# Kernel optimization log

Hardware: AMD Instinct MI355X
Metric: run time of the kernel (lower is better)

Reference implementation:

```python
import jax, jax.numpy as jnp
import numpy as np

N, D_IN, D_HID, D_OUT, E = 8192, 1024, 4096, 1024, 8
N_ACTIVE = max(1, int(E * 0.625))  # 5
TEMP = float(np.e)               # temperature = np.e in source


def setup_inputs() -> dict:
    key = jax.random.key(0)
    ks = jax.random.split(key, 4)
    return {
        "x": jax.random.normal(ks[0], (N, D_IN), jnp.float32),
        "gate_w": jax.random.normal(ks[1], (D_IN, E), jnp.float32) * 0.02,
        "gate_b": jnp.zeros((E,), jnp.float32),
        "w1": jax.random.normal(ks[2], (E, D_IN, D_HID), jnp.float32) * 0.02,
        "b1": jnp.zeros((E, D_HID), jnp.float32),
        "w2": jax.random.normal(ks[3], (E, D_HID, D_OUT), jnp.float32) * 0.02,
        "b2": jnp.zeros((E, D_OUT), jnp.float32),
    }


def reference(x, gate_w, gate_b, w1, b1, w2, b2):
    # Gate: softmax over experts at temperature e, then top-k mask + renormalize
    scores = (x @ gate_w + gate_b) / TEMP                 # [N, E]
    probs = jax.nn.softmax(scores, axis=-1)               # [N, E]
    _, topk_idx = jax.lax.top_k(probs, N_ACTIVE)          # [N, k]
    mask = jax.nn.one_hot(topk_idx, E, dtype=probs.dtype).sum(axis=-2)  # [N, E]
    weights = probs * mask
    weights = weights / (weights.sum(axis=-1, keepdims=True) + 1e-8)
    # Dense all-experts FFN (dropout is eval-mode identity)
    h = jax.nn.relu(jnp.einsum('nd,edh->neh', x, w1) + b1)   # [N, E, d_hid]
    e_out = jnp.einsum('neh,eho->neo', h, w2) + b2           # [N, E, d_out]
    # Camp A (first E/2 experts) added, camp G subtracted: out = out_a - out_g
    sign = jnp.where(jnp.arange(E) < E // 2, 1.0, -1.0)      # [E]
    return jnp.einsum('ne,neo->no', weights * sign, e_out)   # [N, d_out]
```

## Files before the change

### kernel.cpp

```cpp
#include <hip/hip_runtime.h>
#include <hip/hip_bf16.h>
#include <cmath>


typedef _Float16 f16;
typedef _Float16 f16x8 __attribute__((ext_vector_type(8)));
typedef _Float16 f16x4 __attribute__((ext_vector_type(4)));
typedef float f32x4 __attribute__((ext_vector_type(4)));

#define NROWS 8192
#define DIN   1024
#define DHID  4096
#define DOUT  1024
#define NEXP  8

#define OFF_SGATE 0u
#define OFF_XH    262144u
#define OFF_W1T   17039360u
#define OFF_W2T   84148224u
#define OFF_P1    151257088u
#define OFF_HH    184811520u
#define NEED_NE2  319029248ull

__device__ __forceinline__ void gload_lds16(const void* gsrc, void* ldsdst) {
  __builtin_amdgcn_global_load_lds(
      (const __attribute__((address_space(1))) unsigned int*)gsrc,
      (__attribute__((address_space(3))) unsigned int*)ldsdst, 16, 0, 0);
}

__global__ void gate_kernel(const float* __restrict__ x,
                            const float* __restrict__ gw,
                            const float* __restrict__ gb,
                            float* __restrict__ sgate) {
  const int row = blockIdx.x * 4 + (threadIdx.x >> 6);
  const int l = threadIdx.x & 63;
  const float* xr = x + (size_t)row * DIN;
  float acc[8] = {0.f,0.f,0.f,0.f,0.f,0.f,0.f,0.f};
#pragma unroll
  for (int j = 0; j < 16; ++j) {
    const int k = l + 64 * j;
    const float xv = xr[k];
    const float4 g0 = *(const float4*)(gw + (size_t)k * 8);
    const float4 g1 = *(const float4*)(gw + (size_t)k * 8 + 4);
    acc[0] += xv * g0.x; acc[1] += xv * g0.y; acc[2] += xv * g0.z; acc[3] += xv * g0.w;
    acc[4] += xv * g1.x; acc[5] += xv * g1.y; acc[6] += xv * g1.z; acc[7] += xv * g1.w;
  }
#pragma unroll
  for (int off = 32; off > 0; off >>= 1) {
#pragma unroll
    for (int e = 0; e < 8; ++e) acc[e] += __shfl_xor(acc[e], off, 64);
  }
  if (l == 0) {
    const float invT = 0.36787944117144233f;
    float p[8]; float mx = -1e30f;
#pragma unroll
    for (int e = 0; e < 8; ++e) { p[e] = (acc[e] + gb[e]) * invT; mx = fmaxf(mx, p[e]); }
    float S = 0.f;
#pragma unroll
    for (int e = 0; e < 8; ++e) { p[e] = expf(p[e] - mx); S += p[e]; }
    const float inv = 1.0f / S;
#pragma unroll
    for (int e = 0; e < 8; ++e) p[e] *= inv;
    bool keep[8] = {true,true,true,true,true,true,true,true};
    for (int t = 0; t < 3; ++t) {
      float pmin = 1e30f; int mi = -1;
      for (int e = 0; e < 8; ++e)
        if (keep[e] && (p[e] < pmin || (p[e] == pmin && e > mi))) { pmin = p[e]; mi = e; }
      keep[mi] = false;
    }
    float wsum = 0.f;
#pragma unroll
    for (int e = 0; e < 8; ++e) if (keep[e]) wsum += p[e];
    const float rinv = 1.0f / (wsum + 1e-8f);
#pragma unroll
    for (int e = 0; e < 8; ++e) {
      const float wv = keep[e] ? p[e] * rinv : 0.0f;
      sgate[(size_t)row * 8 + e] = (e < 4) ? wv : -wv;
    }
  }
}

__global__ void cvt_x_kernel(const float* __restrict__ x, f16* __restrict__ xh) {
  const size_t i = ((size_t)blockIdx.x * blockDim.x + threadIdx.x) * 4;
  const float4 v = *(const float4*)(x + i);
  f16x4 o = { (f16)v.x, (f16)v.y, (f16)v.z, (f16)v.w };
  *(f16x4*)(xh + i) = o;
}

__global__ void transpose_cvt(const float* __restrict__ in, f16* __restrict__ out,
                              int R, int C) {
  __shared__ float tile[32][33];
  const int e = blockIdx.z;
  const float* ine = in + (size_t)e * R * C;
  f16* oute = out + (size_t)e * R * C;
  const int c0 = blockIdx.x * 32, r0 = blockIdx.y * 32;
  const int tx = threadIdx.x, ty = threadIdx.y;
#pragma unroll
  for (int i = 0; i < 4; ++i)
    tile[ty + i * 8][tx] = ine[(size_t)(r0 + ty + i * 8) * C + c0 + tx];
  __syncthreads();
#pragma unroll
  for (int i = 0; i < 4; ++i)
    oute[(size_t)(c0 + ty + i * 8) * R + r0 + tx] = (f16)tile[tx][ty + i * 8];
}

#define MFMAOP(a_, b_, c_) __builtin_amdgcn_mfma_f32_16x16x32_f16(a_, b_, c_, 0, 0, 0)

template <int EPI>
__global__ __launch_bounds__(512, 2) void gemm8p(
    const f16* __restrict__ A, int lda,
    const f16* __restrict__ B, int ldb, int nt,
    long long khA, long long khB,
    const float* __restrict__ bias,
    f16* __restrict__ outH, int ldc,
    float* outP0, float* outP1, int p1w,
    const float* __restrict__ sgate, int expert, int gx) {
  __shared__ alignas(16) f16 lA[4 * 8192];
  __shared__ alignas(16) f16 lB[4 * 8192];
  const int tid = threadIdx.x;
  const int l = tid & 63, w = tid >> 6;
  const int wr = w >> 2, wc = w & 3;

  const int nwg = gridDim.x, cpx = nwg >> 3;
  const int lg = ((int)blockIdx.x & 7) * cpx + ((int)blockIdx.x >> 3);

  int m0, n0;
  const f16* Aeff = A;
  const f16* Beff = B;
  float* P = nullptr;
  bool pw = false;
  if constexpr (EPI == 1) {
    const int xcd = lg / cpx;
    const int cc = lg - xcd * cpx;
    const int nper = gx >> 3;
    m0 = (cc / nper) * 256;
    n0 = (xcd * nper + (cc % nper)) * 256;
  } else {
    const int xx = lg >> 5, cc = lg & 31;
    const int kh = xx >> 2;
    n0 = (xx & 3) * 256;
    m0 = cc * 256;
    Aeff = A + (size_t)kh * (size_t)khA;
    Beff = B + (size_t)kh * (size_t)khB;
    P = kh ? outP1 : outP0;
    pw = (p1w != 0);
  }

  const int srow = tid >> 3;
  const int sxc = (tid & 7) ^ (srow & 7);
  const f16* pA = Aeff + (size_t)(m0 + srow) * lda + sxc * 8;
  const f16* pB = Beff + (size_t)(n0 + srow) * ldb + sxc * 8;
  f16* const dA = lA + w * 512;
  f16* const dB = lB + w * 512;

#define STG_A(slot, h, tk) do { \
    const f16* s_ = pA + (size_t)(h) * 128 * lda + (size_t)(tk) * 64; \
    gload_lds16(s_,            dA + (slot) * 8192); \
    gload_lds16(s_ + 64 * lda, dA + (slot) * 8192 + 4096); \
  } while (0)
#define STG_B(slot, h, tk) do { \
    const f16* s_ = pB + (size_t)(h) * 128 * ldb + (size_t)(tk) * 64; \
    gload_lds16(s_,            dB + (slot) * 8192); \
    gload_lds16(s_ + 64 * ldb, dB + (slot) * 8192 + 4096); \
  } while (0)

  const int cg = l >> 4, xr = l & 7;
  const int ok0 = ((cg ^ xr) << 4);
  const int ok1 = (((4 + cg) ^ xr) << 4);
  const char* const baA = (const char*)lA + (l & 15) * 128;
  const char* const baB = (const char*)lB + (wc & 1) * 8192 + (l & 15) * 128;

#define RDA(CA, f, o) (*(const f16x8*)(baA + ((CA) + wr) * 16384 + (f) * 2048 + (o)))
#define RDB(CB, g, o) (*(const f16x8*)(baB + ((CB) + (wc >> 1)) * 16384 + (g) * 2048 + (o)))

#define SYNC() do { __builtin_amdgcn_sched_barrier(0); \
    __builtin_amdgcn_s_barrier(); \
    __builtin_amdgcn_sched_barrier(0); } while (0)
#define ENDPH() do { __builtin_amdgcn_s_setprio(0); \
    __builtin_amdgcn_sched_barrier(0); \
    __builtin_amdgcn_s_barrier(); \
    __builtin_amdgcn_sched_barrier(0); } while (0)
#define VM6() do { __builtin_amdgcn_sched_barrier(0); \
    asm volatile("s_waitcnt vmcnt(6)"); \
    __builtin_amdgcn_sched_barrier(0); } while (0)
#define VM0() do { __builtin_amdgcn_sched_barrier(0); \
    asm volatile("s_waitcnt vmcnt(0)"); \
    __builtin_amdgcn_sched_barrier(0); } while (0)
#define MM(f, g, ar, br) acc[f][g] = MFMAOP(ar, br, acc[f][g])

  f32x4 acc[8][4] = {};
  f16x8 fa0, fa1, fa2, fa3;
  f16x8 ga0, ga1, ga2, ga3;
  f16x8 b00, b10, b20, b30;
  f16x8 b01, b11, b21, b31;

#define TILEBODY(T, CA, CB, SB1, SB0n, SA0n, SA1n) do { \
     \
    fa0 = RDA(CA, 0, ok0); fa1 = RDA(CA, 1, ok0); \
    fa2 = RDA(CA, 2, ok0); fa3 = RDA(CA, 3, ok0); \
    b00 = RDB(CB, 0, ok0); b10 = RDB(CB, 1, ok0); \
    b20 = RDB(CB, 2, ok0); b30 = RDB(CB, 3, ok0); \
    if ((T) + 1 < nt) STG_B(SB1, 1, (T) + 1); \
    SYNC(); \
    __builtin_amdgcn_s_setprio(1); \
    MM(0,0,fa0,b00); MM(0,1,fa0,b10); MM(0,2,fa0,b20); MM(0,3,fa0,b30); \
    MM(1,0,fa1,b00); MM(1,1,fa1,b10); MM(1,2,fa1,b20); MM(1,3,fa1,b30); \
    MM(2,0,fa2,b00); MM(2,1,fa2,b10); MM(2,2,fa2,b20); MM(2,3,fa2,b30); \
    MM(3,0,fa3,b00); MM(3,1,fa3,b10); MM(3,2,fa3,b20); MM(3,3,fa3,b30); \
    ENDPH(); \
     \
    ga0 = RDA(CA, 0, ok1); ga1 = RDA(CA, 1, ok1); \
    ga2 = RDA(CA, 2, ok1); ga3 = RDA(CA, 3, ok1); \
    b01 = RDB(CB, 0, ok1); b11 = RDB(CB, 1, ok1); \
    b21 = RDB(CB, 2, ok1); b31 = RDB(CB, 3, ok1); \
    SYNC(); \
    __builtin_amdgcn_s_setprio(1); \
    MM(0,0,ga0,b01); MM(0,1,ga0,b11); MM(0,2,ga0,b21); MM(0,3,ga0,b31); \
    MM(1,0,ga1,b01); MM(1,1,ga1,b11); MM(1,2,ga1,b21); MM(1,3,ga1,b31); \
    MM(2,0,ga2,b01); MM(2,1,ga2,b11); MM(2,2,ga2,b21); MM(2,3,ga2,b31); \
    MM(3,0,ga3,b01); MM(3,1,ga3,b11); MM(3,2,ga3,b21); MM(3,3,ga3,b31); \
    ENDPH(); \
     \
    fa0 = RDA(CA, 4, ok0); fa1 = RDA(CA, 5, ok0); \
    fa2 = RDA(CA, 6, ok0); fa3 = RDA(CA, 7, ok0); \
    ga0 = RDA(CA, 4, ok1); ga1 = RDA(CA, 5, ok1); \
    ga2 = RDA(CA, 6, ok1); ga3 = RDA(CA, 7, ok1); \
    if ((T) + 2 < nt) STG_B(SB0n, 0, (T) + 2); \
    SYNC(); \
    __builtin_amdgcn_s_setprio(1); \
    MM(4,0,fa0,b00); MM(4,1,fa0,b10); MM(4,2,fa0,b20); MM(4,3,fa0,b30); \
    MM(5,0,fa1,b00); MM(5,1,fa1,b10); MM(5,2,fa1,b20); MM(5,3,fa1,b30); \
    MM(6,0,fa2,b00); MM(6,1,fa2,b10); MM(6,2,fa2,b20); MM(6,3,fa2,b30); \
    MM(7,0,fa3,b00); MM(7,1,fa3,b10); MM(7,2,fa3,b20); MM(7,3,fa3,b30); \
    ENDPH(); \
     \
    if ((T) + 2 < nt) { STG_A(SA0n, 0, (T) + 2); STG_A(SA1n, 1, (T) + 2); \
                        VM6(); } \
    else { VM0(); } \
    SYNC(); \
    __builtin_amdgcn_s_setprio(1); \
    MM(4,0,ga0,b01); MM(4,1,ga0,b11); MM(4,2,ga0,b21); MM(4,3,ga0,b31); \
    MM(5,0,ga1,b01); MM(5,1,ga1,b11); MM(5,2,ga1,b21); MM(5,3,ga1,b31); \
    MM(6,0,ga2,b01); MM(6,1,ga2,b11); MM(6,2,ga2,b21); MM(6,3,ga2,b31); \
    MM(7,0,ga3,b01); MM(7,1,ga3,b11); MM(7,2,ga3,b21); MM(7,3,ga3,b31); \
    ENDPH(); \
  } while (0)

  STG_A(0, 0, 0); STG_B(0, 0, 0); STG_A(1, 1, 0); STG_B(1, 1, 0);
  STG_A(2, 0, 1); STG_B(2, 0, 1); STG_A(3, 1, 1);
  __builtin_amdgcn_sched_barrier(0);
  asm volatile("s_waitcnt vmcnt(6)");
  __builtin_amdgcn_sched_barrier(0);
  __builtin_amdgcn_s_barrier();
  __builtin_amdgcn_sched_barrier(0);

  for (int t = 0; t < nt; t += 2) {
    TILEBODY(t,     0, 0, 3, 0, 0, 1);
    TILEBODY(t + 1, 2, 2, 1, 2, 2, 3);
  }
  __builtin_amdgcn_sched_barrier(0);
  asm volatile("s_waitcnt vmcnt(0)");
  __builtin_amdgcn_sched_barrier(0);

  if constexpr (EPI == 1) {
#pragma unroll
    for (int mi = 0; mi < 8; ++mi)
#pragma unroll
      for (int r = 0; r < 4; ++r) {
        const int row = m0 + wr * 128 + mi * 16 + (l >> 4) * 4 + r;
        const float sg = sgate[(size_t)row * 8 + expert];
#pragma unroll
        for (int ni = 0; ni < 4; ++ni) {
          const int col = n0 + wc * 64 + ni * 16 + (l & 15);
          const float v = acc[mi][ni][r] + bias[col];
          outH[(size_t)row * ldc + col] = (f16)(fmaxf(v, 0.0f) * sg);
        }
      }
  } else {
    float* const scr = (w < 4) ? (float*)lA + w * 4096
                               : (float*)lB + (w - 4) * 4096;
    const int hl = l >> 4, ll = l & 15;
#pragma unroll
    for (int p = 0; p < 2; ++p) {
#pragma unroll
      for (int mi4 = 0; mi4 < 4; ++mi4)
#pragma unroll
        for (int r = 0; r < 4; ++r) {
          const int rowl = mi4 * 16 + hl * 4 + r;
#pragma unroll
          for (int ni = 0; ni < 4; ++ni)
            scr[rowl * 64 + ni * 16 + ll] = acc[p * 4 + mi4][ni][r];
        }
#pragma unroll
      for (int i = 0; i < 16; ++i) {
        const int rowl = hl + i * 4;
        f32x4 v = *(const f32x4*)(scr + rowl * 64 + ll * 4);
        const int row = m0 + wr * 128 + p * 64 + rowl;
        const int col = n0 + wc * 64 + ll * 4;
        f32x4* gp = (f32x4*)(P + (size_t)row * 1024 + col);
        if (!pw) {
          const f32x4 g = *gp;
          v[0] += g[0]; v[1] += g[1]; v[2] += g[2]; v[3] += g[3];
        }
        *gp = v;
      }
    }
  }
#undef STG_A
#undef STG_B
#undef RDA
#undef RDB
#undef SYNC
#undef ENDPH
#undef VM6
#undef VM0
#undef MM
#undef TILEBODY
}

template <bool WITHP>
__global__ void finalize_out(const float* p0,
                             const float* __restrict__ p1,
                             const float* __restrict__ sgate,
                             const float* __restrict__ b2,
                             float* out) {
  const int i = blockIdx.x * 256 + threadIdx.x;
  const int n = i >> 8, c4 = i & 255;
  float4 a = make_float4(0.f, 0.f, 0.f, 0.f);
  if constexpr (WITHP) {
    const float4 u = ((const float4*)p0)[i];
    const float4 v = ((const float4*)p1)[i];
    a.x = u.x + v.x; a.y = u.y + v.y; a.z = u.z + v.z; a.w = u.w + v.w;
  }
  const float* sg = sgate + (size_t)n * 8;
#pragma unroll
  for (int e = 0; e < 8; ++e) {
    const float s = sg[e];
    const float4 bv = ((const float4*)(b2 + (size_t)e * 1024))[c4];
    a.x += s * bv.x; a.y += s * bv.y; a.z += s * bv.z; a.w += s * bv.w;
  }
  ((float4*)out)[i] = a;
}

extern "C" void kernel_launch(void* const* d_in, const int* in_sizes, int n_in,
                              void* d_out, int out_size, void* d_ws, size_t ws_size,
                              hipStream_t stream) {
  const float* x  = (const float*)d_in[0];
  const float* gw = (const float*)d_in[1];
  const float* gb = (const float*)d_in[2];
  const float* w1 = (const float*)d_in[3];
  const float* b1 = (const float*)d_in[4];
  const float* w2 = (const float*)d_in[5];
  const float* b2 = (const float*)d_in[6];
  float* out = (float*)d_out;

  char* ws = (char*)d_ws;
  float* sgate = (float*)(ws + OFF_SGATE);
  f16* xh  = (f16*)(ws + OFF_XH);
  f16* w1t = (f16*)(ws + OFF_W1T);
  f16* w2t = (f16*)(ws + OFF_W2T);
  float* p1 = (float*)(ws + OFF_P1);
  f16* hh  = (f16*)(ws + OFF_HH);

  const int NE = (ws_size >= NEED_NE2) ? 2 : 1;
  const int ngrp = NEXP / NE;

  gate_kernel<<<NROWS / 4, 256, 0, stream>>>(x, gw, gb, sgate);
  cvt_x_kernel<<<(NROWS * DIN) / (256 * 4), 256, 0, stream>>>(x, xh);
  transpose_cvt<<<dim3(DHID / 32, DIN / 32, NEXP), dim3(32, 8), 0, stream>>>(w1, w1t, DIN, DHID);
  transpose_cvt<<<dim3(DOUT / 32, DHID / 32, NEXP), dim3(32, 8), 0, stream>>>(w2, w2t, DHID, DOUT);

  const long long khA = (long long)NE * 2048;
  const long long khB = (NE == 2) ? (long long)DOUT * DHID
                                  : 2048LL;
  const int nt2 = NE * 32;
  for (int g = 0; g < ngrp; ++g) {
    for (int ei = 0; ei < NE; ++ei) {
      const int e = g * NE + ei;
      gemm8p<1><<<512, 512, 0, stream>>>(
          xh, DIN, w1t + (size_t)e * DHID * DIN, DIN, DIN / 64,
          0, 0,
          b1 + (size_t)e * DHID, hh + (size_t)ei * DHID, NE * DHID,
          nullptr, nullptr, 0, sgate, e, DHID / 256);
    }
    gemm8p<2><<<256, 512, 0, stream>>>(
        hh, NE * DHID, w2t + (size_t)g * NE * DOUT * DHID, DHID, nt2,
        khA, khB,
        nullptr, nullptr, 0, out, p1, (g == 0) ? 1 : 0, nullptr, 0, 0);
  }
  finalize_out<true><<<(NROWS * DOUT) / (256 * 4), 256, 0, stream>>>(
      out, p1, sgate, b2, out);
}
```

Baseline: 1.442 ms.

## Software-pipeline LDS fragment reads one phase ahead of MFMA in GEMM mainloop

Restructures the GEMM inner loop so the LDS reads for the next phase are issued before the current phase's MFMAs. This adds more fragment registers (16 A-fragment registers instead of 8), and the first fragments of the next tile are prefetched after the end-of-tile barrier. Several of the block barriers before compute phases are removed or replaced with lgkmcnt waits. The goal is to hide LDS read latency behind matrix-core work and cut barrier stalls. The cost is higher VGPR pressure, which may lower occupancy, and a subtler synchronisation scheme that has to stay race-free.

```diff
diff --git a/kernel.cpp b/kernel.cpp
--- a/kernel.cpp
+++ b/kernel.cpp
@@ -173,94 +173,98 @@
 #define RDA(CA, f, o) (*(const f16x8*)(baA + ((CA) + wr) * 16384 + (f) * 2048 + (o)))
 #define RDB(CB, g, o) (*(const f16x8*)(baB + ((CB) + (wc >> 1)) * 16384 + (g) * 2048 + (o)))
 
-#define SYNC() do { __builtin_amdgcn_sched_barrier(0); \
-    __builtin_amdgcn_s_barrier(); \
-    __builtin_amdgcn_sched_barrier(0); } while (0)
-#define ENDPH() do { __builtin_amdgcn_s_setprio(0); \
-    __builtin_amdgcn_sched_barrier(0); \
-    __builtin_amdgcn_s_barrier(); \
-    __builtin_amdgcn_sched_barrier(0); } while (0)
-#define VM6() do { __builtin_amdgcn_sched_barrier(0); \
-    asm volatile("s_waitcnt vmcnt(6)"); \
-    __builtin_amdgcn_sched_barrier(0); } while (0)
-#define VM0() do { __builtin_amdgcn_sched_barrier(0); \
-    asm volatile("s_waitcnt vmcnt(0)"); \
-    __builtin_amdgcn_sched_barrier(0); } while (0)
+#define SB0() __builtin_amdgcn_sched_barrier(0)
+#define ENDPH() do { __builtin_amdgcn_s_setprio(0); SB0(); \
+    __builtin_amdgcn_s_barrier(); SB0(); } while (0)
+#define LGKM0() do { SB0(); asm volatile("s_waitcnt lgkmcnt(0)"); SB0(); } while (0)
+#define VM6() do { SB0(); asm volatile("s_waitcnt vmcnt(6)"); SB0(); } while (0)
+#define VM0() do { SB0(); asm volatile("s_waitcnt vmcnt(0)"); SB0(); } while (0)
 #define MM(f, g, ar, br) acc[f][g] = MFMAOP(ar, br, acc[f][g])
 
   f32x4 acc[8][4] = {};
-  f16x8 fa0, fa1, fa2, fa3;
-  f16x8 ga0, ga1, ga2, ga3;
+  f16x8 a00, a01, a02, a03;
+  f16x8 a10, a11, a12, a13;
+  f16x8 a20, a21, a22, a23;
+  f16x8 a30, a31, a32, a33;
   f16x8 b00, b10, b20, b30;
   f16x8 b01, b11, b21, b31;
 
-#define TILEBODY(T, CA, CB, SB1, SB0n, SA0n, SA1n) do { \
+#define TILEBODY(T, CA, CB, SB1, SB0n, SA0n, SA1n, CAn, CBn) do { \
      \
-    fa0 = RDA(CA, 0, ok0); fa1 = RDA(CA, 1, ok0); \
-    fa2 = RDA(CA, 2, ok0); fa3 = RDA(CA, 3, ok0); \
-    b00 = RDB(CB, 0, ok0); b10 = RDB(CB, 1, ok0); \
-    b20 = RDB(CB, 2, ok0); b30 = RDB(CB, 3, ok0); \
     if ((T) + 1 < nt) STG_B(SB1, 1, (T) + 1); \
-    SYNC(); \
+    a10 = RDA(CA, 0, ok1); a11 = RDA(CA, 1, ok1); \
+    a12 = RDA(CA, 2, ok1); a13 = RDA(CA, 3, ok1); \
+    b01 = RDB(CB, 0, ok1); b11 = RDB(CB, 1, ok1); \
+    b21 = RDB(CB, 2, ok1); b31 = RDB(CB, 3, ok1); \
+    SB0(); \
     __builtin_amdgcn_s_setprio(1); \
-    MM(0,0,fa0,b00); MM(0,1,fa0,b10); MM(0,2,fa0,b20); MM(0,3,fa0,b30); \
-    MM(1,0,fa1,b00); MM(1,1,fa1,b10); MM(1,2,fa1,b20); MM(1,3,fa1,b30); \
-    MM(2,0,fa2,b00); MM(2,1,fa2,b10); MM(2,2,fa2,b20); MM(2,3,fa2,b30); \
-    MM(3,0,fa3,b00); MM(3,1,fa3,b10); MM(3,2,fa3,b20); MM(3,3,fa3,b30); \
+    MM(0,0,a00,b00); MM(0,1,a00,b10); MM(0,2,a00,b20); MM(0,3,a00,b30); \
+    MM(1,0,a01,b00); MM(1,1,a01,b10); MM(1,2,a01,b20); MM(1,3,a01,b30); \
+    MM(2,0,a02,b00); MM(2,1,a02,b10); MM(2,2,a02,b20); MM(2,3,a02,b30); \
+    MM(3,0,a03,b00); MM(3,1,a03,b10); MM(3,2,a03,b20); MM(3,3,a03,b30); \
     ENDPH(); \
      \
-    ga0 = RDA(CA, 0, ok1); ga1 = RDA(CA, 1, ok1); \
-    ga2 = RDA(CA, 2, ok1); ga3 = RDA(CA, 3, ok1); \
-    b01 = RDB(CB, 0, ok1); b11 = RDB(CB, 1, ok1); \
-    b21 = RDB(CB, 2, ok1); b31 = RDB(CB, 3, ok1); \
-    SYNC(); \
+    a20 = RDA(CA, 4, ok0); a21 = RDA(CA, 5, ok0); \
+    a22 = RDA(CA, 6, ok0); a23 = RDA(CA, 7, ok0); \
+    a30 = RDA(CA, 4, ok1); a31 = RDA(CA, 5, ok1); \
+    a32 = RDA(CA, 6, ok1); a33 = RDA(CA, 7, ok1); \
+    SB0(); \
     __builtin_amdgcn_s_setprio(1); \
-    MM(0,0,ga0,b01); MM(0,1,ga0,b11); MM(0,2,ga0,b21); MM(0,3,ga0,b31); \
-    MM(1,0,ga1,b01); MM(1,1,ga1,b11); MM(1,2,ga1,b21); MM(1,3,ga1,b31); \
-    MM(2,0,ga2,b01); MM(2,1,ga2,b11); MM(2,2,ga2,b21); MM(2,3,ga2,b31); \
-    MM(3,0,ga3,b01); MM(3,1,ga3,b11); MM(3,2,ga3,b21); MM(3,3,ga3,b31); \
+    MM(0,0,a10,b01); MM(0,1,a10,b11); MM(0,2,a10,b21); MM(0,3,a10,b31); \
+    MM(1,0,a11,b01); MM(1,1,a11,b11); MM(1,2,a11,b21); MM(1,3,a11,b31); \
+    MM(2,0,a12,b01); MM(2,1,a12,b11); MM(2,2,a12,b21); MM(2,3,a12,b31); \
+    MM(3,0,a13,b01); MM(3,1,a13,b11); MM(3,2,a13,b21); MM(3,3,a13,b31); \
     ENDPH(); \
      \
-    fa0 = RDA(CA, 4, ok0); fa1 = RDA(CA, 5, ok0); \
-    fa2 = RDA(CA, 6, ok0); fa3 = RDA(CA, 7, ok0); \
-    ga0 = RDA(CA, 4, ok1); ga1 = RDA(CA, 5, ok1); \
-    ga2 = RDA(CA, 6, ok1); ga3 = RDA(CA, 7, ok1); \
     if ((T) + 2 < nt) STG_B(SB0n, 0, (T) + 2); \
-    SYNC(); \
+    LGKM0(); \
     __builtin_amdgcn_s_setprio(1); \
-    MM(4,0,fa0,b00); MM(4,1,fa0,b10); MM(4,2,fa0,b20); MM(4,3,fa0,b30); \
-    MM(5,0,fa1,b00); MM(5,1,fa1,b10); MM(5,2,fa1,b20); MM(5,3,fa1,b30); \
-    MM(6,0,fa2,b00); MM(6,1,fa2,b10); MM(6,2,fa2,b20); MM(6,3,fa2,b30); \
-    MM(7,0,fa3,b00); MM(7,1,fa3,b10); MM(7,2,fa3,b20); MM(7,3,fa3,b30); \
+    MM(4,0,a20,b00); MM(4,1,a20,b10); MM(4,2,a20,b20); MM(4,3,a20,b30); \
+    MM(5,0,a21,b00); MM(5,1,a21,b10); MM(5,2,a21,b20); MM(5,3,a21,b30); \
+    MM(6,0,a22,b00); MM(6,1,a22,b10); MM(6,2,a22,b20); MM(6,3,a22,b30); \
+    MM(7,0,a23,b00); MM(7,1,a23,b10); MM(7,2,a23,b20); MM(7,3,a23,b30); \
     ENDPH(); \
      \
     if ((T) + 2 < nt) { STG_A(SA0n, 0, (T) + 2); STG_A(SA1n, 1, (T) + 2); \
                         VM6(); } \
     else { VM0(); } \
-    SYNC(); \
+    __builtin_amdgcn_s_barrier(); \
+    SB0(); \
+    if ((T) + 1 < nt) { \
+      a00 = RDA(CAn, 0, ok0); a01 = RDA(CAn, 1, ok0); \
+      a02 = RDA(CAn, 2, ok0); a03 = RDA(CAn, 3, ok0); \
+      b00 = RDB(CBn, 0, ok0); b10 = RDB(CBn, 1, ok0); \
+      b20 = RDB(CBn, 2, ok0); b30 = RDB(CBn, 3, ok0); \
+    } \
+    SB0(); \
     __builtin_amdgcn_s_setprio(1); \
-    MM(4,0,ga0,b01); MM(4,1,ga0,b11); MM(4,2,ga0,b21); MM(4,3,ga0,b31); \
-    MM(5,0,ga1,b01); MM(5,1,ga1,b11); MM(5,2,ga1,b21); MM(5,3,ga1,b31); \
-    MM(6,0,ga2,b01); MM(6,1,ga2,b11); MM(6,2,ga2,b21); MM(6,3,ga2,b31); \
-    MM(7,0,ga3,b01); MM(7,1,ga3,b11); MM(7,2,ga3,b21); MM(7,3,ga3,b31); \
+    MM(4,0,a30,b01); MM(4,1,a30,b11); MM(4,2,a30,b21); MM(4,3,a30,b31); \
+    MM(5,0,a31,b01); MM(5,1,a31,b11); MM(5,2,a31,b21); MM(5,3,a31,b31); \
+    MM(6,0,a32,b01); MM(6,1,a32,b11); MM(6,2,a32,b21); MM(6,3,a32,b31); \
+    MM(7,0,a33,b01); MM(7,1,a33,b11); MM(7,2,a33,b21); MM(7,3,a33,b31); \
     ENDPH(); \
   } while (0)
 
   STG_A(0, 0, 0); STG_B(0, 0, 0); STG_A(1, 1, 0); STG_B(1, 1, 0);
   STG_A(2, 0, 1); STG_B(2, 0, 1); STG_A(3, 1, 1);
-  __builtin_amdgcn_sched_barrier(0);
+  SB0();
   asm volatile("s_waitcnt vmcnt(6)");
-  __builtin_amdgcn_sched_barrier(0);
+  SB0();
   __builtin_amdgcn_s_barrier();
-  __builtin_amdgcn_sched_barrier(0);
+  SB0();
+  a00 = RDA(0, 0, ok0); a01 = RDA(0, 1, ok0);
+  a02 = RDA(0, 2, ok0); a03 = RDA(0, 3, ok0);
+  b00 = RDB(0, 0, ok0); b10 = RDB(0, 1, ok0);
+  b20 = RDB(0, 2, ok0); b30 = RDB(0, 3, ok0);
+  SB0();
 
   for (int t = 0; t < nt; t += 2) {
-    TILEBODY(t,     0, 0, 3, 0, 0, 1);
-    TILEBODY(t + 1, 2, 2, 1, 2, 2, 3);
-  }
-  __builtin_amdgcn_sched_barrier(0);
+    TILEBODY(t,     0, 0, 3, 0, 0, 1, 2, 2);
+    TILEBODY(t + 1, 2, 2, 1, 2, 2, 3, 0, 0);
+  }
+  SB0();
   asm volatile("s_waitcnt vmcnt(0)");
-  __builtin_amdgcn_sched_barrier(0);
+  SB0();
 
   if constexpr (EPI == 1) {
 #pragma unroll
@@ -310,8 +314,9 @@
 #undef STG_B
 #undef RDA
 #undef RDB
-#undef SYNC
+#undef SB0
 #undef ENDPH
+#undef LGKM0
 #undef VM6
 #undef VM0
 #undef MM
```

After: 1.976 ms. +37.0%, slower.

## Route only top-k selected tokens through each expert via gathered indices

Applied to the files above, without the earlier changes.

The gate kernel now builds per-expert token index lists with atomic counters. Each expert's first GEMM gathers only its selected rows and skips tiles beyond the padded count, and the second GEMM scatter-adds into output rows. Since each token keeps 5 of 8 experts, this cuts matmul work relative to dense all-expert compute. It adds a zero-init pass, atomics, non-contiguous row gathers and read-modify-write scatter accumulation, and it drops the two-expert batching path.

```diff
diff --git a/kernel.cpp b/kernel.cpp
--- a/kernel.cpp
+++ b/kernel.cpp
@@ -15,12 +15,13 @@
 #define NEXP  8
 
 #define OFF_SGATE 0u
-#define OFF_XH    262144u
-#define OFF_W1T   17039360u
-#define OFF_W2T   84148224u
-#define OFF_P1    151257088u
-#define OFF_HH    184811520u
-#define NEED_NE2  319029248ull
+#define OFF_CNT   262144u
+#define OFF_IDX   266240u
+#define OFF_XH    528384u
+#define OFF_W1T   17305600u
+#define OFF_W2T   84414464u
+#define OFF_P1    151523328u
+#define OFF_HH    185077760u
 
 __device__ __forceinline__ void gload_lds16(const void* gsrc, void* ldsdst) {
   __builtin_amdgcn_global_load_lds(
@@ -28,10 +29,21 @@
       (__attribute__((address_space(3))) unsigned int*)ldsdst, 16, 0, 0);
 }
 
+__global__ void zero_init(float* __restrict__ out, float* __restrict__ p1,
+                          int* __restrict__ cnt) {
+  const size_t i = (size_t)blockIdx.x * 256 + threadIdx.x;
+  const float4 z = make_float4(0.f, 0.f, 0.f, 0.f);
+  ((float4*)out)[i] = z;
+  ((float4*)p1)[i] = z;
+  if (blockIdx.x == 0 && threadIdx.x < 8) cnt[threadIdx.x] = 0;
+}
+
 __global__ void gate_kernel(const float* __restrict__ x,
                             const float* __restrict__ gw,
                             const float* __restrict__ gb,
-                            float* __restrict__ sgate) {
+                            float* __restrict__ sgate,
+                            int* __restrict__ cnt,
+                            int* __restrict__ idx) {
   const int row = blockIdx.x * 4 + (threadIdx.x >> 6);
   const int l = threadIdx.x & 63;
   const float* xr = x + (size_t)row * DIN;
@@ -77,6 +89,11 @@
       const float wv = keep[e] ? p[e] * rinv : 0.0f;
       sgate[(size_t)row * 8 + e] = (e < 4) ? wv : -wv;
     }
+    for (int e = 0; e < 8; ++e)
+      if (keep[e]) {
+        const int pos = atomicAdd(&cnt[e], 1);
+        idx[e * NROWS + pos] = row;
+      }
   }
 }
 
@@ -110,10 +127,10 @@
 __global__ __launch_bounds__(512, 2) void gemm8p(
     const f16* __restrict__ A, int lda,
     const f16* __restrict__ B, int ldb, int nt,
-    long long khA, long long khB,
+    const int* __restrict__ idx_e, const int* __restrict__ cntp,
     const float* __restrict__ bias,
     f16* __restrict__ outH, int ldc,
-    float* outP0, float* outP1, int p1w,
+    float* outP0, float* outP1,
     const float* __restrict__ sgate, int expert, int gx) {
   __shared__ alignas(16) f16 lA[4 * 8192];
   __shared__ alignas(16) f16 lB[4 * 8192];
@@ -124,11 +141,13 @@
   const int nwg = gridDim.x, cpx = nwg >> 3;
   const int lg = ((int)blockIdx.x & 7) * cpx + ((int)blockIdx.x >> 3);
 
+  const int Me = cntp[expert];
+  const int Mpad = (Me + 255) & ~255;
+
   int m0, n0;
   const f16* Aeff = A;
   const f16* Beff = B;
   float* P = nullptr;
-  bool pw = false;
   if constexpr (EPI == 1) {
     const int xcd = lg / cpx;
     const int cc = lg - xcd * cpx;
@@ -140,23 +159,36 @@
     const int kh = xx >> 2;
     n0 = (xx & 3) * 256;
     m0 = cc * 256;
-    Aeff = A + (size_t)kh * (size_t)khA;
-    Beff = B + (size_t)kh * (size_t)khB;
+    Aeff = A + kh * 2048;
+    Beff = B + kh * 2048;
     P = kh ? outP1 : outP0;
-    pw = (p1w != 0);
-  }
+  }
+  if (m0 >= Mpad) return;
 
   const int srow = tid >> 3;
   const int sxc = (tid & 7) ^ (srow & 7);
-  const f16* pA = Aeff + (size_t)(m0 + srow) * lda + sxc * 8;
+  const f16 *pA00, *pA01, *pA10, *pA11;
+  if constexpr (EPI == 1) {
+    const int r00 = m0 + srow,       r01 = m0 + 64 + srow;
+    const int r10 = m0 + 128 + srow, r11 = m0 + 192 + srow;
+    pA00 = A + (size_t)((r00 < Me) ? idx_e[r00] : 0) * lda + sxc * 8;
+    pA01 = A + (size_t)((r01 < Me) ? idx_e[r01] : 0) * lda + sxc * 8;
+    pA10 = A + (size_t)((r10 < Me) ? idx_e[r10] : 0) * lda + sxc * 8;
+    pA11 = A + (size_t)((r11 < Me) ? idx_e[r11] : 0) * lda + sxc * 8;
+  } else {
+    pA00 = Aeff + (size_t)(m0 + srow) * lda + sxc * 8;
+    pA01 = pA00 + (size_t)64 * lda;
+    pA10 = pA00 + (size_t)128 * lda;
+    pA11 = pA00 + (size_t)192 * lda;
+  }
   const f16* pB = Beff + (size_t)(n0 + srow) * ldb + sxc * 8;
   f16* const dA = lA + w * 512;
   f16* const dB = lB + w * 512;
 
 #define STG_A(slot, h, tk) do { \
-    const f16* s_ = pA + (size_t)(h) * 128 * lda + (size_t)(tk) * 64; \
-    gload_lds16(s_,            dA + (slot) * 8192); \
-    gload_lds16(s_ + 64 * lda, dA + (slot) * 8192 + 4096); \
+    const size_t kb = (size_t)(tk) * 64; \
+    gload_lds16(((h) ? pA10 : pA00) + kb, dA + (slot) * 8192); \
+    gload_lds16(((h) ? pA11 : pA01) + kb, dA + (slot) * 8192 + 4096); \
   } while (0)
 #define STG_B(slot, h, tk) do { \
     const f16* s_ = pB + (size_t)(h) * 128 * ldb + (size_t)(tk) * 64; \
@@ -173,19 +205,12 @@
 #define RDA(CA, f, o) (*(const f16x8*)(baA + ((CA) + wr) * 16384 + (f) * 2048 + (o)))
 #define RDB(CB, g, o) (*(const f16x8*)(baB + ((CB) + (wc >> 1)) * 16384 + (g) * 2048 + (o)))
 
-#define SYNC() do { __builtin_amdgcn_sched_barrier(0); \
-    __builtin_amdgcn_s_barrier(); \
-    __builtin_amdgcn_sched_barrier(0); } while (0)
-#define ENDPH() do { __builtin_amdgcn_s_setprio(0); \
-    __builtin_amdgcn_sched_barrier(0); \
-    __builtin_amdgcn_s_barrier(); \
-    __builtin_amdgcn_sched_barrier(0); } while (0)
-#define VM6() do { __builtin_amdgcn_sched_barrier(0); \
-    asm volatile("s_waitcnt vmcnt(6)"); \
-    __builtin_amdgcn_sched_barrier(0); } while (0)
-#define VM0() do { __builtin_amdgcn_sched_barrier(0); \
-    asm volatile("s_waitcnt vmcnt(0)"); \
-    __builtin_amdgcn_sched_barrier(0); } while (0)
+#define SB0() __builtin_amdgcn_sched_barrier(0)
+#define SYNC() do { SB0(); __builtin_amdgcn_s_barrier(); SB0(); } while (0)
+#define ENDPH() do { __builtin_amdgcn_s_setprio(0); SB0(); \
+    __builtin_amdgcn_s_barrier(); SB0(); } while (0)
+#define VM6() do { SB0(); asm volatile("s_waitcnt vmcnt(6)"); SB0(); } while (0)
+#define VM0() do { SB0(); asm volatile("s_waitcnt vmcnt(0)"); SB0(); } while (0)
 #define MM(f, g, ar, br) acc[f][g] = MFMAOP(ar, br, acc[f][g])
 
   f32x4 acc[8][4] = {};
@@ -248,32 +273,33 @@
 
   STG_A(0, 0, 0); STG_B(0, 0, 0); STG_A(1, 1, 0); STG_B(1, 1, 0);
   STG_A(2, 0, 1); STG_B(2, 0, 1); STG_A(3, 1, 1);
-  __builtin_amdgcn_sched_barrier(0);
+  SB0();
   asm volatile("s_waitcnt vmcnt(6)");
-  __builtin_amdgcn_sched_barrier(0);
+  SB0();
   __builtin_amdgcn_s_barrier();
-  __builtin_amdgcn_sched_barrier(0);
+  SB0();
 
   for (int t = 0; t < nt; t += 2) {
     TILEBODY(t,     0, 0, 3, 0, 0, 1);
     TILEBODY(t + 1, 2, 2, 1, 2, 2, 3);
   }
-  __builtin_amdgcn_sched_barrier(0);
+  SB0();
   asm volatile("s_waitcnt vmcnt(0)");
-  __builtin_amdgcn_sched_barrier(0);
+  SB0();
 
   if constexpr (EPI == 1) {
 #pragma unroll
     for (int mi = 0; mi < 8; ++mi)
 #pragma unroll
       for (int r = 0; r < 4; ++r) {
-        const int row = m0 + wr * 128 + mi * 16 + (l >> 4) * 4 + r;
-        const float sg = sgate[(size_t)row * 8 + expert];
+        const int slot = m0 + wr * 128 + mi * 16 + (l >> 4) * 4 + r;
+        const int grow = (slot < Me) ? idx_e[slot] : 0;
+        const float sg = sgate[(size_t)grow * 8 + expert];
 #pragma unroll
         for (int ni = 0; ni < 4; ++ni) {
           const int col = n0 + wc * 64 + ni * 16 + (l & 15);
           const float v = acc[mi][ni][r] + bias[col];
-          outH[(size_t)row * ldc + col] = (f16)(fmaxf(v, 0.0f) * sg);
+          outH[(size_t)slot * ldc + col] = (f16)(fmaxf(v, 0.0f) * sg);
         }
       }
   } else {
@@ -294,15 +320,16 @@
 #pragma unroll
       for (int i = 0; i < 16; ++i) {
         const int rowl = hl + i * 4;
-        f32x4 v = *(const f32x4*)(scr + rowl * 64 + ll * 4);
-        const int row = m0 + wr * 128 + p * 64 + rowl;
-        const int col = n0 + wc * 64 + ll * 4;
-        f32x4* gp = (f32x4*)(P + (size_t)row * 1024 + col);
-        if (!pw) {
+        const int slot = m0 + wr * 128 + p * 64 + rowl;
+        if (slot < Me) {
+          f32x4 v = *(const f32x4*)(scr + rowl * 64 + ll * 4);
+          const int grow = idx_e[slot];
+          const int col = n0 + wc * 64 + ll * 4;
+          f32x4* gp = (f32x4*)(P + (size_t)grow * 1024 + col);
           const f32x4 g = *gp;
           v[0] += g[0]; v[1] += g[1]; v[2] += g[2]; v[3] += g[3];
+          *gp = v;
         }
-        *gp = v;
       }
     }
   }
@@ -310,6 +337,7 @@
 #undef STG_B
 #undef RDA
 #undef RDB
+#undef SB0
 #undef SYNC
 #undef ENDPH
 #undef VM6
@@ -318,7 +346,6 @@
 #undef TILEBODY
 }
 
-template <bool WITHP>
 __global__ void finalize_out(const float* p0,
                              const float* __restrict__ p1,
                              const float* __restrict__ sgate,
@@ -326,12 +353,9 @@
                              float* out) {
   const int i = blockIdx.x * 256 + threadIdx.x;
   const int n = i >> 8, c4 = i & 255;
-  float4 a = make_float4(0.f, 0.f, 0.f, 0.f);
-  if constexpr (WITHP) {
-    const float4 u = ((const float4*)p0)[i];
-    const float4 v = ((const float4*)p1)[i];
-    a.x = u.x + v.x; a.y = u.y + v.y; a.z = u.z + v.z; a.w = u.w + v.w;
-  }
+  const float4 u = ((const float4*)p0)[i];
+  const float4 v = ((const float4*)p1)[i];
+  float4 a = make_float4(u.x + v.x, u.y + v.y, u.z + v.z, u.w + v.w);
   const float* sg = sgate + (size_t)n * 8;
 #pragma unroll
   for (int e = 0; e < 8; ++e) {
@@ -356,38 +380,32 @@
 
   char* ws = (char*)d_ws;
   float* sgate = (float*)(ws + OFF_SGATE);
+  int*   cnt   = (int*)(ws + OFF_CNT);
+  int*   idx   = (int*)(ws + OFF_IDX);
   f16* xh  = (f16*)(ws + OFF_XH);
   f16* w1t = (f16*)(ws + OFF_W1T);
   f16* w2t = (f16*)(ws + OFF_W2T);
   float* p1 = (float*)(ws + OFF_P1);
   f16* hh  = (f16*)(ws + OFF_HH);
 
-  const int NE = (ws_size >= NEED_NE2) ? 2 : 1;
-  const int ngrp = NEXP / NE;
-
-  gate_kernel<<<NROWS / 4, 256, 0, stream>>>(x, gw, gb, sgate);
+  zero_init<<<(NROWS * DOUT) / (256 * 4), 256, 0, stream>>>(out, p1, cnt);
+  gate_kernel<<<NROWS / 4, 256, 0, stream>>>(x, gw, gb, sgate, cnt, idx);
   cvt_x_kernel<<<(NROWS * DIN) / (256 * 4), 256, 0, stream>>>(x, xh);
   transpose_cvt<<<dim3(DHID / 32, DIN / 32, NEXP), dim3(32, 8), 0, stream>>>(w1, w1t, DIN, DHID);
   transpose_cvt<<<dim3(DOUT / 32, DHID / 32, NEXP), dim3(32, 8), 0, stream>>>(w2, w2t, DHID, DOUT);
 
-  const long long khA = (long long)NE * 2048;
-  const long long khB = (NE == 2) ? (long long)DOUT * DHID
-                                  : 2048LL;
-  const int nt2 = NE * 32;
-  for (int g = 0; g < ngrp; ++g) {
-    for (int ei = 0; ei < NE; ++ei) {
-      const int e = g * NE + ei;
-      gemm8p<1><<<512, 512, 0, stream>>>(
-          xh, DIN, w1t + (size_t)e * DHID * DIN, DIN, DIN / 64,
-          0, 0,
-          b1 + (size_t)e * DHID, hh + (size_t)ei * DHID, NE * DHID,
-          nullptr, nullptr, 0, sgate, e, DHID / 256);
-    }
+  for (int e = 0; e < NEXP; ++e) {
+    gemm8p<1><<<512, 512, 0, stream>>>(
+        xh, DIN, w1t + (size_t)e * DHID * DIN, DIN, DIN / 64,
+        idx + (size_t)e * NROWS, cnt,
+        b1 + (size_t)e * DHID, hh, DHID,
+        nullptr, nullptr, sgate, e, DHID / 256);
     gemm8p<2><<<256, 512, 0, stream>>>(
-        hh, NE * DHID, w2t + (size_t)g * NE * DOUT * DHID, DHID, nt2,
-        khA, khB,
-        nullptr, nullptr, 0, out, p1, (g == 0) ? 1 : 0, nullptr, 0, 0);
-  }
-  finalize_out<true><<<(NROWS * DOUT) / (256 * 4), 256, 0, stream>>>(
+        hh, DHID, w2t + (size_t)e * DOUT * DHID, DHID, 2048 / 64,
+        idx + (size_t)e * NROWS, cnt,
+        nullptr, nullptr, 0,
+        out, p1, sgate, e, DOUT / 256);
+  }
+  finalize_out<<<(NROWS * DOUT) / (256 * 4), 256, 0, stream>>>(
       out, p1, sgate, b2, out);
 }
```

Result: slower. 2.041 ms (+41.5%).
